# Performance work log

Measured on AMD Instinct MI355X. Metric: run time of the kernel, lower is better.

The kernel has to match this reference:

```python
import jax, jax.numpy as jnp
import numpy as np

N_USERS = 100000
N_ENT = 100000
DIM = 64
HID = 128
E = 1600000
B = 8192


def _renorm(emb, max_norm=1.0):
    # torch nn.Embedding(max_norm=1): rows are rescaled to norm <= max_norm on lookup
    n = jnp.linalg.norm(emb, axis=-1, keepdims=True)
    return emb * jnp.minimum(1.0, max_norm / jnp.maximum(n, 1e-12))


def _gcn_conv(x, W, b, src, dst, n):
    # PyG GCNConv: h = x W; add self-loops; sym-normalized scatter-add; + bias
    h = x @ W  # [n, out]
    deg = jax.ops.segment_sum(jnp.ones(src.shape, jnp.float32), dst, num_segments=n) + 1.0  # self-loop
    dinv = jax.lax.rsqrt(deg)
    norm = (dinv[src] * dinv[dst])[:, None]  # [E,1]
    out = jax.ops.segment_sum(h[src] * norm, dst, num_segments=n)
    out = out + h * (1.0 / deg)[:, None]  # self-loop term: deg^-1/2 * deg^-1/2 = 1/deg
    return out + b


def setup_inputs() -> dict:
    key = jax.random.key(0)
    ks = jax.random.split(key, 8)
    return {
        "u": jax.random.randint(ks[0], (B,), 0, N_USERS),
        "i": jax.random.randint(ks[1], (B,), 0, N_ENT),
        "edges": jax.random.randint(ks[2], (2, E), 0, N_ENT),
        "user_emb": jax.random.normal(ks[3], (N_USERS, DIM), jnp.float32) * 0.1,
        "entity_emb": jax.random.normal(ks[4], (N_ENT, DIM), jnp.float32) * 0.1,
        "W1": jax.random.normal(ks[5], (DIM, HID), jnp.float32) * (1.0 / np.sqrt(DIM)),
        "b1": jnp.zeros((HID,), jnp.float32),
        "W2": jax.random.normal(ks[6], (HID, DIM), jnp.float32) * (1.0 / np.sqrt(HID)),
        "b2": jnp.zeros((DIM,), jnp.float32),
    }


def reference(u, i, edges, user_emb, entity_emb, W1, b1, W2, b2):
    src, dst = edges[0], edges[1]
    n = entity_emb.shape[0]
    x = _renorm(entity_emb)  # entitys(all_entitys_indexes) with max_norm=1
    x = jax.nn.relu(_gcn_conv(x, W1, b1, src, dst, n))  # dropout = identity (eval)
    x = _gcn_conv(x, W2, b2, src, dst, n)
    items = x[i]  # [B, DIM]
    users = _renorm(user_emb)[u]  # [B, DIM]
    uv = jnp.sum(users * items, axis=1)
    return jax.nn.sigmoid(uv)
```

## Files before the change

### kernel.cpp

```cpp
#include <hip/hip_runtime.h>
#include <hip/hip_bf16.h>
#include <math.h>

constexpr int N_ENT = 100000;
constexpr int NEDGE = 1600000;
constexpr int BATCH = 8192;
constexpr int NBLK_SCAN = (N_ENT + 255) / 256;

constexpr int NBUCK   = 256;
constexpr int KNODE   = 391;
constexpr int TILE    = 4096;
constexpr int NTILE   = (NEDGE + TILE - 1) / TILE;
constexpr int BUCKCAP = 8192;

constexpr int NBLK_G = (N_ENT + 63) / 64;
constexpr int ZROWS  = NBLK_G * 64;

typedef __attribute__((ext_vector_type(8))) short bf16x8;
typedef __attribute__((ext_vector_type(4))) float f32x4;

__device__ inline unsigned short f2b(float x) {
    unsigned int u = __float_as_uint(x);
    unsigned int r = (u + 0x7fffu + ((u >> 16) & 1u)) >> 16;
    return (unsigned short)r;
}
__device__ inline float b2f(unsigned short h) {
    return __uint_as_float(((unsigned int)h) << 16);
}
__device__ inline float blo(unsigned int p) { return __uint_as_float(p << 16); }
__device__ inline float bhi(unsigned int p) { return __uint_as_float(p & 0xffff0000u); }


__global__ __launch_bounds__(256) void prep_k(const float* __restrict__ emb,
                                              const int* __restrict__ degi,
                                              float* __restrict__ dinv,
                                              unsigned short* __restrict__ emb_b) {
    int gt   = blockIdx.x * 256 + threadIdx.x;
    int n    = gt >> 6;
    int lane = threadIdx.x & 63;
    if (n > N_ENT) return;
    if (n == N_ENT) { emb_b[(size_t)n * 64 + lane] = 0; return; }
    float v = emb[(size_t)n * 64 + lane];
    float s = v * v;
#pragma unroll
    for (int o = 32; o > 0; o >>= 1) s += __shfl_xor(s, o, 64);
    float nrm = sqrtf(s);
    float sc  = nrm > 1.0f ? 1.0f / nrm : 1.0f;
    float dv  = 1.0f / sqrtf((float)(degi[n] + 1));
    if (lane == 0) dinv[n] = dv;
    emb_b[(size_t)n * 64 + lane] = f2b(sc * dv * v);
}

__global__ __launch_bounds__(256) void ginit_k(int* __restrict__ gcursor) {
    gcursor[threadIdx.x] = threadIdx.x * BUCKCAP;
}

__global__ __launch_bounds__(256) void packw_k(const float* __restrict__ W1g,
                                               const float* __restrict__ W2g,
                                               uint4* __restrict__ w1p,
                                               uint4* __restrict__ w2p) {
    int t = blockIdx.x * 256 + threadIdx.x;
    int e    = t & 1023;
    int lane = e & 63, cs = e >> 6;
    int li   = lane & 15, quad = lane >> 4;
    unsigned short v[8];
    if (t < 1024) {
        int ct = cs >> 1, s = cs & 1;
        int kb = s * 32 + quad * 8;
        int n  = ct * 16 + li;
#pragma unroll
        for (int j = 0; j < 8; ++j) v[j] = f2b(W1g[(kb + j) * 128 + n]);
        uint4 p;
        p.x = (unsigned)v[0] | ((unsigned)v[1] << 16);
        p.y = (unsigned)v[2] | ((unsigned)v[3] << 16);
        p.z = (unsigned)v[4] | ((unsigned)v[5] << 16);
        p.w = (unsigned)v[6] | ((unsigned)v[7] << 16);
        w1p[e] = p;
    } else {
        int ct = cs >> 2, s = cs & 3;
        int kb = s * 32 + quad * 8;
        int n  = ct * 16 + li;
#pragma unroll
        for (int j = 0; j < 8; ++j) v[j] = f2b(W2g[(kb + j) * 64 + n]);
        uint4 p;
        p.x = (unsigned)v[0] | ((unsigned)v[1] << 16);
        p.y = (unsigned)v[2] | ((unsigned)v[3] << 16);
        p.z = (unsigned)v[4] | ((unsigned)v[5] << 16);
        p.w = (unsigned)v[6] | ((unsigned)v[7] << 16);
        w2p[e] = p;
    }
}

__global__ __launch_bounds__(256) void bin_k(const int* __restrict__ edges,
                                             int* __restrict__ gcursor,
                                             unsigned int* __restrict__ temp) {
    __shared__ int cnt[NBUCK];
    __shared__ int gb[NBUCK];
    __shared__ int off[NBUCK];
    int tid  = threadIdx.x;
    int base = blockIdx.x * TILE;
    int sv[16], dv[16], bv[16];
    cnt[tid] = 0;
    __syncthreads();
#pragma unroll
    for (int i = 0; i < 16; ++i) {
        int e = base + i * 256 + tid;
        if (e < NEDGE) {
            sv[i] = edges[e];
            dv[i] = edges[NEDGE + e];
            bv[i] = dv[i] / KNODE;
            atomicAdd(&cnt[bv[i]], 1);
        } else {
            bv[i] = -1;
        }
    }
    __syncthreads();
    if (cnt[tid] > 0) gb[tid] = atomicAdd(&gcursor[tid], cnt[tid]);
    off[tid] = 0;
    __syncthreads();
#pragma unroll
    for (int i = 0; i < 16; ++i) {
        int b = bv[i];
        if (b >= 0) {
            int p  = atomicAdd(&off[b], 1);
            int dl = dv[i] - b * KNODE;
            temp[gb[b] + p] = ((unsigned int)sv[i] << 9) | (unsigned int)dl;
        }
    }
}

__global__ __launch_bounds__(256) void count_k(const unsigned int* __restrict__ temp,
                                               const int* __restrict__ gcursor,
                                               int* __restrict__ degi) {
    __shared__ int cnt[KNODE];
    int b     = blockIdx.x;
    int node0 = b * KNODE;
    int nn    = N_ENT - node0; if (nn > KNODE) nn = KNODE;
    for (int i = threadIdx.x; i < KNODE; i += 256) cnt[i] = 0;
    __syncthreads();
    int tbeg = b * BUCKCAP;
    int tend = gcursor[b];
    for (int idx = tbeg + threadIdx.x; idx < tend; idx += 256)
        atomicAdd(&cnt[temp[idx] & 511u], 1);
    __syncthreads();
    for (int i = threadIdx.x; i < nn; i += 256) degi[node0 + i] = cnt[i];
}

__global__ __launch_bounds__(256) void scan_partials(const int* __restrict__ degi,
                                                     int* __restrict__ partials) {
    __shared__ int ws[4];
    int i = blockIdx.x * 256 + threadIdx.x;
    int v = (i < N_ENT) ? degi[i] : 0;
#pragma unroll
    for (int o = 32; o > 0; o >>= 1) v += __shfl_xor(v, o, 64);
    if ((threadIdx.x & 63) == 0) ws[threadIdx.x >> 6] = v;
    __syncthreads();
    if (threadIdx.x == 0) partials[blockIdx.x] = ws[0] + ws[1] + ws[2] + ws[3];
}

__global__ __launch_bounds__(512) void scan_offsets(int* __restrict__ partials,
                                                    int* __restrict__ row_start) {
    __shared__ int ts[512];
    int t = threadIdx.x;
    int v = (t < NBLK_SCAN) ? partials[t] : 0;
    ts[t] = v;
    __syncthreads();
    for (int off = 1; off < 512; off <<= 1) {
        int x = (t >= off) ? ts[t - off] : 0;
        __syncthreads();
        ts[t] += x;
        __syncthreads();
    }
    if (t < NBLK_SCAN) partials[t] = ts[t] - v;
    if (t == 0) row_start[N_ENT] = NEDGE;
}

__global__ __launch_bounds__(256) void scan_apply(const int* __restrict__ degi,
                                                  const int* __restrict__ partials,
                                                  int* __restrict__ row_start) {
    __shared__ int ts[256];
    int t = threadIdx.x;
    int i = blockIdx.x * 256 + t;
    int v = (i < N_ENT) ? degi[i] : 0;
    ts[t] = v;
    __syncthreads();
    for (int off = 1; off < 256; off <<= 1) {
        int x = (t >= off) ? ts[t - off] : 0;
        __syncthreads();
        ts[t] += x;
        __syncthreads();
    }
    if (i < N_ENT) row_start[i] = ts[t] - v + partials[blockIdx.x];
}

__global__ __launch_bounds__(256) void unbin_k(const unsigned int* __restrict__ temp,
                                               const int* __restrict__ gcursor,
                                               const int* __restrict__ row_start,
                                               int* __restrict__ srcs) {
    __shared__ int cur[KNODE];
    int b     = blockIdx.x;
    int node0 = b * KNODE;
    int nn    = N_ENT - node0; if (nn > KNODE) nn = KNODE;
    for (int i = threadIdx.x; i < nn; i += 256) cur[i] = row_start[node0 + i];
    __syncthreads();
    int tbeg = b * BUCKCAP;
    int tend = gcursor[b];
    for (int idx = tbeg + threadIdx.x; idx < tend; idx += 256) {
        unsigned int v = temp[idx];
        int dl = (int)(v & 511u);
        int s  = (int)(v >> 9);
        int pos = atomicAdd(&cur[dl], 1);
        srcs[pos] = s;
    }
}

__global__ __launch_bounds__(256) void reduce1_k(const int* __restrict__ row_start,
                                                 const int* __restrict__ srcs,
                                                 const unsigned short* __restrict__ emb_b,
                                                 const float* __restrict__ dinv,
                                                 unsigned short* __restrict__ zb) {
    int gt   = blockIdx.x * 256 + threadIdx.x;
    int dst  = gt >> 6;
    int lane = threadIdx.x & 63;
    int sub  = lane >> 4;
    int li   = lane & 15;
    int beg = row_start[dst];
    int end = row_start[dst + 1];
    float4 acc = make_float4(0.f, 0.f, 0.f, 0.f);
    for (int base = beg; base < end; base += 64) {
        int cnt = end - base; if (cnt > 64) cnt = 64;
        int s_v = (base + lane < end) ? srcs[base + lane] : N_ENT;
        for (int jj = 0; jj < cnt; jj += 16) {
            int s0 = __shfl(s_v, jj + sub,      64);
            int s1 = __shfl(s_v, jj + 4 + sub,  64);
            int s2 = __shfl(s_v, jj + 8 + sub,  64);
            int s3 = __shfl(s_v, jj + 12 + sub, 64);
            uint2 p0 = *(const uint2*)(emb_b + (size_t)s0 * 64 + li * 4);
            uint2 p1 = *(const uint2*)(emb_b + (size_t)s1 * 64 + li * 4);
            uint2 p2 = *(const uint2*)(emb_b + (size_t)s2 * 64 + li * 4);
            uint2 p3 = *(const uint2*)(emb_b + (size_t)s3 * 64 + li * 4);
            acc.x += blo(p0.x) + blo(p1.x) + blo(p2.x) + blo(p3.x);
            acc.y += bhi(p0.x) + bhi(p1.x) + bhi(p2.x) + bhi(p3.x);
            acc.z += blo(p0.y) + blo(p1.y) + blo(p2.y) + blo(p3.y);
            acc.w += bhi(p0.y) + bhi(p1.y) + bhi(p2.y) + bhi(p3.y);
        }
    }
    acc.x += __shfl_xor(acc.x, 16, 64); acc.y += __shfl_xor(acc.y, 16, 64);
    acc.z += __shfl_xor(acc.z, 16, 64); acc.w += __shfl_xor(acc.w, 16, 64);
    acc.x += __shfl_xor(acc.x, 32, 64); acc.y += __shfl_xor(acc.y, 32, 64);
    acc.z += __shfl_xor(acc.z, 32, 64); acc.w += __shfl_xor(acc.w, 32, 64);
    if (lane < 16) {
        uint2 po = *(const uint2*)(emb_b + (size_t)dst * 64 + li * 4);
        float dv = dinv[dst];
        unsigned int h0 = f2b(dv * (acc.x + blo(po.x)));
        unsigned int h1 = f2b(dv * (acc.y + bhi(po.x)));
        unsigned int h2 = f2b(dv * (acc.z + blo(po.y)));
        unsigned int h3 = f2b(dv * (acc.w + bhi(po.y)));
        uint2 p;
        p.x = h0 | (h1 << 16);
        p.y = h2 | (h3 << 16);
        *(uint2*)(zb + (size_t)dst * 64 + li * 4) = p;
    }
}

__global__ __launch_bounds__(256) void mlp_k(const unsigned short* __restrict__ zb,
                                             const uint4* __restrict__ w1p,
                                             const float* __restrict__ b1,
                                             const uint4* __restrict__ w2p,
                                             const float* __restrict__ dinv,
                                             unsigned short* __restrict__ h2b) {
    __shared__ unsigned short y1s[4][16 * 136];
    __shared__ unsigned short h2s[4][16 * 64];
    int tid  = threadIdx.x;
    int w    = tid >> 6, lane = tid & 63;
    int li   = lane & 15, quad = lane >> 4;
    int r0   = blockIdx.x * 64 + w * 16;
    uint4 a0u = *(const uint4*)(zb + (size_t)(r0 + li) * 64 + quad * 8);
    uint4 a1u = *(const uint4*)(zb + (size_t)(r0 + li) * 64 + 32 + quad * 8);
    bf16x8 a0 = *(bf16x8*)&a0u;
    bf16x8 a1 = *(bf16x8*)&a1u;
    unsigned short* ys = y1s[w];
#pragma unroll
    for (int ct = 0; ct < 8; ++ct) {
        uint4 b0u = w1p[(ct * 2 + 0) * 64 + lane];
        uint4 b1u = w1p[(ct * 2 + 1) * 64 + lane];
        f32x4 acc = {0.f, 0.f, 0.f, 0.f};
        acc = __builtin_amdgcn_mfma_f32_16x16x32_bf16(a0, *(bf16x8*)&b0u, acc, 0, 0, 0);
        acc = __builtin_amdgcn_mfma_f32_16x16x32_bf16(a1, *(bf16x8*)&b1u, acc, 0, 0, 0);
        float bias = b1[ct * 16 + li];
#pragma unroll
        for (int r = 0; r < 4; ++r)
            ys[(quad * 4 + r) * 136 + ct * 16 + li] = f2b(fmaxf(acc[r] + bias, 0.f));
    }
    __syncthreads();
    bf16x8 a2[4];
#pragma unroll
    for (int s = 0; s < 4; ++s) {
        uint4 au = *(const uint4*)(ys + li * 136 + s * 32 + quad * 8);
        a2[s] = *(bf16x8*)&au;
    }
    float dvr[4];
#pragma unroll
    for (int r = 0; r < 4; ++r) {
        int grow = r0 + quad * 4 + r;
        dvr[r] = (grow < N_ENT) ? dinv[grow] : 0.f;
    }
    unsigned short* hs = h2s[w];
#pragma unroll
    for (int ct = 0; ct < 4; ++ct) {
        f32x4 acc = {0.f, 0.f, 0.f, 0.f};
#pragma unroll
        for (int s = 0; s < 4; ++s) {
            uint4 bu = w2p[(ct * 4 + s) * 64 + lane];
            acc = __builtin_amdgcn_mfma_f32_16x16x32_bf16(a2[s], *(bf16x8*)&bu, acc, 0, 0, 0);
        }
#pragma unroll
        for (int r = 0; r < 4; ++r)
            hs[(quad * 4 + r) * 64 + ct * 16 + li] = f2b(acc[r] * dvr[r]);
    }
    __syncthreads();
#pragma unroll
    for (int q = 0; q < 2; ++q) {
        int t4   = lane * 2 + q;
        int rl   = t4 >> 3;
        int c0   = (t4 & 7) * 8;
        int grow = r0 + rl;
        if (grow < N_ENT) {
            *(uint4*)(h2b + (size_t)grow * 64 + c0) = *(const uint4*)(hs + rl * 64 + c0);
        } else if (grow == N_ENT) {
            uint4 zz; zz.x = 0u; zz.y = 0u; zz.z = 0u; zz.w = 0u;
            *(uint4*)(h2b + (size_t)grow * 64 + c0) = zz;
        }
    }
}

__global__ __launch_bounds__(256) void reduce2f_k(const int* __restrict__ u,
                                                  const int* __restrict__ iidx,
                                                  const float* __restrict__ uemb,
                                                  const int* __restrict__ row_start,
                                                  const int* __restrict__ srcs,
                                                  const unsigned short* __restrict__ h2b,
                                                  const float* __restrict__ dinv,
                                                  const float* __restrict__ b2,
                                                  float* __restrict__ out) {
    int gt   = blockIdx.x * 256 + threadIdx.x;
    int b    = gt >> 6;
    int lane = threadIdx.x & 63;
    int sub  = lane >> 4;
    int li   = lane & 15;
    int dst = iidx[b];
    int beg = row_start[dst];
    int end = row_start[dst + 1];
    float4 acc = make_float4(0.f, 0.f, 0.f, 0.f);
    for (int base = beg; base < end; base += 64) {
        int cnt = end - base; if (cnt > 64) cnt = 64;
        int s_v = (base + lane < end) ? srcs[base + lane] : N_ENT;
        for (int jj = 0; jj < cnt; jj += 16) {
            int s0 = __shfl(s_v, jj + sub,      64);
            int s1 = __shfl(s_v, jj + 4 + sub,  64);
            int s2 = __shfl(s_v, jj + 8 + sub,  64);
            int s3 = __shfl(s_v, jj + 12 + sub, 64);
            uint2 p0 = *(const uint2*)(h2b + (size_t)s0 * 64 + li * 4);
            uint2 p1 = *(const uint2*)(h2b + (size_t)s1 * 64 + li * 4);
            uint2 p2 = *(const uint2*)(h2b + (size_t)s2 * 64 + li * 4);
            uint2 p3 = *(const uint2*)(h2b + (size_t)s3 * 64 + li * 4);
            acc.x += blo(p0.x) + blo(p1.x) + blo(p2.x) + blo(p3.x);
            acc.y += bhi(p0.x) + bhi(p1.x) + bhi(p2.x) + bhi(p3.x);
            acc.z += blo(p0.y) + blo(p1.y) + blo(p2.y) + blo(p3.y);
            acc.w += bhi(p0.y) + bhi(p1.y) + bhi(p2.y) + bhi(p3.y);
        }
    }
    acc.x += __shfl_xor(acc.x, 16, 64); acc.y += __shfl_xor(acc.y, 16, 64);
    acc.z += __shfl_xor(acc.z, 16, 64); acc.w += __shfl_xor(acc.w, 16, 64);
    acc.x += __shfl_xor(acc.x, 32, 64); acc.y += __shfl_xor(acc.y, 32, 64);
    acc.z += __shfl_xor(acc.z, 32, 64); acc.w += __shfl_xor(acc.w, 32, 64);
    float s1 = 0.f, s2 = 0.f;
    if (lane < 16) {
        uint2 po = *(const uint2*)(h2b + (size_t)dst * 64 + li * 4);
        float dv = dinv[dst];
        float4 bb = *(const float4*)(b2 + li * 4);
        float4 z2v;
        z2v.x = dv * (acc.x + blo(po.x)) + bb.x;
        z2v.y = dv * (acc.y + bhi(po.x)) + bb.y;
        z2v.z = dv * (acc.z + blo(po.y)) + bb.z;
        z2v.w = dv * (acc.w + bhi(po.y)) + bb.w;
        float4 ue = *(const float4*)(uemb + (size_t)u[b] * 64 + li * 4);
        s1 = ue.x * ue.x + ue.y * ue.y + ue.z * ue.z + ue.w * ue.w;
        s2 = ue.x * z2v.x + ue.y * z2v.y + ue.z * z2v.z + ue.w * z2v.w;
    }
#pragma unroll
    for (int o = 8; o > 0; o >>= 1) {
        s1 += __shfl_xor(s1, o, 64);
        s2 += __shfl_xor(s2, o, 64);
    }
    if (lane == 0) {
        float nrm = sqrtf(s1);
        float sc  = nrm > 1.0f ? 1.0f / nrm : 1.0f;
        float uv  = s2 * sc;
        out[b] = 1.0f / (1.0f + expf(-uv));
    }
}

extern "C" void kernel_launch(void* const* d_in, const int* in_sizes, int n_in,
                              void* d_out, int out_size, void* d_ws, size_t ws_size,
                              hipStream_t stream) {
    const int*   u          = (const int*)d_in[0];
    const int*   iidx       = (const int*)d_in[1];
    const int*   edges      = (const int*)d_in[2];
    const float* user_emb   = (const float*)d_in[3];
    const float* entity_emb = (const float*)d_in[4];
    const float* W1         = (const float*)d_in[5];
    const float* b1         = (const float*)d_in[6];
    const float* W2         = (const float*)d_in[7];
    const float* b2         = (const float*)d_in[8];
    float*       out        = (float*)d_out;

    char* ws = (char*)d_ws;
    int*            degi      = (int*)           (ws);
    float*          dinv      = (float*)         (ws + 100000u * 4);
    int*            row_start = (int*)           (ws + 200000u * 4);
    int*            gcursor   = (int*)           (ws + 300004u * 4);
    int*            partials  = (int*)           (ws + 300264u * 4);
    uint4*          w1p       = (uint4*)         (ws + 300656u * 4);
    uint4*          w2p       = (uint4*)         (ws + 304752u * 4);
    int*            srcs      = (int*)           (ws + 308848u * 4);
    unsigned short* emb_b     = (unsigned short*)(ws + 1908848u * 4);
    unsigned short* zb        = (unsigned short*)(ws + 3508864u * 4);
    unsigned short* h2b       = (unsigned short*)(ws + 6711936u * 4);
    unsigned int*   temp      = (unsigned int*)  (ws + 8311968u * 4);

    ginit_k<<<1, 256, 0, stream>>>(gcursor);
    packw_k<<<8, 256, 0, stream>>>(W1, W2, w1p, w2p);
    bin_k<<<NTILE, 256, 0, stream>>>(edges, gcursor, temp);
    count_k<<<NBUCK, 256, 0, stream>>>(temp, gcursor, degi);

    prep_k<<<N_ENT * 64 / 256 + 1, 256, 0, stream>>>(entity_emb, degi, dinv, emb_b);

    scan_partials<<<NBLK_SCAN, 256, 0, stream>>>(degi, partials);
    scan_offsets<<<1, 512, 0, stream>>>(partials, row_start);
    scan_apply<<<NBLK_SCAN, 256, 0, stream>>>(degi, partials, row_start);

    unbin_k<<<NBUCK, 256, 0, stream>>>(temp, gcursor, row_start, srcs);

    reduce1_k<<<N_ENT * 64 / 256, 256, 0, stream>>>(row_start, srcs, emb_b, dinv, zb);
    mlp_k<<<NBLK_G, 256, 0, stream>>>(zb, w1p, b1, w2p, dinv, h2b);

    reduce2f_k<<<BATCH * 64 / 256, 256, 0, stream>>>(u, iidx, user_emb, row_start,
                                                     srcs, h2b, dinv, b2, out);
}
```

Before: 244.4 us.

## Split bf16 embeddings into two column planes and run reduce1 as two passes

The bf16 normalized entity embeddings and the first aggregation output are now stored as two planes of 32 columns each instead of interleaved 64-column rows. reduce1 launches twice as many blocks, and each pass gathers only one 64-byte half-row per source, so the gathered working set per pass fits in cache better and there is more parallelism. mlp_k reads its two K-halves from the two planes. The cost is re-reading the CSR indices and row_start twice, plus more wavefronts each doing half the arithmetic.

New measurement: 251.6 us. 2.9% more time.

```diff
diff --git a/kernel.cpp b/kernel.cpp
--- a/kernel.cpp
+++ b/kernel.cpp
@@ -15,6 +15,10 @@
 
 constexpr int NBLK_G = (N_ENT + 63) / 64;
 constexpr int ZROWS  = NBLK_G * 64;
+
+constexpr int    NBLK_R1 = N_ENT * 64 / 256;
+constexpr size_t EPLANE  = (size_t)(N_ENT + 1) * 32;
+constexpr size_t ZPLANE  = (size_t)ZROWS * 32;
 
 typedef __attribute__((ext_vector_type(8))) short bf16x8;
 typedef __attribute__((ext_vector_type(4))) float f32x4;
@@ -39,7 +43,9 @@
     int n    = gt >> 6;
     int lane = threadIdx.x & 63;
     if (n > N_ENT) return;
-    if (n == N_ENT) { emb_b[(size_t)n * 64 + lane] = 0; return; }
+    int plane = lane >> 5;
+    int cp    = lane & 31;
+    if (n == N_ENT) { emb_b[(size_t)plane * EPLANE + (size_t)n * 32 + cp] = 0; return; }
     float v = emb[(size_t)n * 64 + lane];
     float s = v * v;
 #pragma unroll
@@ -48,7 +54,7 @@
     float sc  = nrm > 1.0f ? 1.0f / nrm : 1.0f;
     float dv  = 1.0f / sqrtf((float)(degi[n] + 1));
     if (lane == 0) dinv[n] = dv;
-    emb_b[(size_t)n * 64 + lane] = f2b(sc * dv * v);
+    emb_b[(size_t)plane * EPLANE + (size_t)n * 32 + cp] = f2b(sc * dv * v);
 }
 
 __global__ __launch_bounds__(256) void ginit_k(int* __restrict__ gcursor) {
@@ -219,14 +225,16 @@
                                                  const unsigned short* __restrict__ emb_b,
                                                  const float* __restrict__ dinv,
                                                  unsigned short* __restrict__ zb) {
-    int gt   = blockIdx.x * 256 + threadIdx.x;
+    int pass = (blockIdx.x >= NBLK_R1) ? 1 : 0;
+    int gt   = (blockIdx.x - pass * NBLK_R1) * 256 + threadIdx.x;
     int dst  = gt >> 6;
     int lane = threadIdx.x & 63;
     int sub  = lane >> 4;
     int li   = lane & 15;
+    const unsigned short* eb = emb_b + (size_t)pass * EPLANE;
     int beg = row_start[dst];
     int end = row_start[dst + 1];
-    float4 acc = make_float4(0.f, 0.f, 0.f, 0.f);
+    float accx = 0.f, accy = 0.f;
     for (int base = beg; base < end; base += 64) {
         int cnt = end - base; if (cnt > 64) cnt = 64;
         int s_v = (base + lane < end) ? srcs[base + lane] : N_ENT;
@@ -235,31 +243,23 @@
             int s1 = __shfl(s_v, jj + 4 + sub,  64);
             int s2 = __shfl(s_v, jj + 8 + sub,  64);
             int s3 = __shfl(s_v, jj + 12 + sub, 64);
-            uint2 p0 = *(const uint2*)(emb_b + (size_t)s0 * 64 + li * 4);
-            uint2 p1 = *(const uint2*)(emb_b + (size_t)s1 * 64 + li * 4);
-            uint2 p2 = *(const uint2*)(emb_b + (size_t)s2 * 64 + li * 4);
-            uint2 p3 = *(const uint2*)(emb_b + (size_t)s3 * 64 + li * 4);
-            acc.x += blo(p0.x) + blo(p1.x) + blo(p2.x) + blo(p3.x);
-            acc.y += bhi(p0.x) + bhi(p1.x) + bhi(p2.x) + bhi(p3.x);
-            acc.z += blo(p0.y) + blo(p1.y) + blo(p2.y) + blo(p3.y);
-            acc.w += bhi(p0.y) + bhi(p1.y) + bhi(p2.y) + bhi(p3.y);
-        }
-    }
-    acc.x += __shfl_xor(acc.x, 16, 64); acc.y += __shfl_xor(acc.y, 16, 64);
-    acc.z += __shfl_xor(acc.z, 16, 64); acc.w += __shfl_xor(acc.w, 16, 64);
-    acc.x += __shfl_xor(acc.x, 32, 64); acc.y += __shfl_xor(acc.y, 32, 64);
-    acc.z += __shfl_xor(acc.z, 32, 64); acc.w += __shfl_xor(acc.w, 32, 64);
+            unsigned int p0 = *(const unsigned int*)(eb + (size_t)s0 * 32 + li * 2);
+            unsigned int p1 = *(const unsigned int*)(eb + (size_t)s1 * 32 + li * 2);
+            unsigned int p2 = *(const unsigned int*)(eb + (size_t)s2 * 32 + li * 2);
+            unsigned int p3 = *(const unsigned int*)(eb + (size_t)s3 * 32 + li * 2);
+            accx += blo(p0) + blo(p1) + blo(p2) + blo(p3);
+            accy += bhi(p0) + bhi(p1) + bhi(p2) + bhi(p3);
+        }
+    }
+    accx += __shfl_xor(accx, 16, 64); accy += __shfl_xor(accy, 16, 64);
+    accx += __shfl_xor(accx, 32, 64); accy += __shfl_xor(accy, 32, 64);
     if (lane < 16) {
-        uint2 po = *(const uint2*)(emb_b + (size_t)dst * 64 + li * 4);
+        unsigned int po = *(const unsigned int*)(eb + (size_t)dst * 32 + li * 2);
         float dv = dinv[dst];
-        unsigned int h0 = f2b(dv * (acc.x + blo(po.x)));
-        unsigned int h1 = f2b(dv * (acc.y + bhi(po.x)));
-        unsigned int h2 = f2b(dv * (acc.z + blo(po.y)));
-        unsigned int h3 = f2b(dv * (acc.w + bhi(po.y)));
-        uint2 p;
-        p.x = h0 | (h1 << 16);
-        p.y = h2 | (h3 << 16);
-        *(uint2*)(zb + (size_t)dst * 64 + li * 4) = p;
+        unsigned int h0 = f2b(dv * (accx + blo(po)));
+        unsigned int h1 = f2b(dv * (accy + bhi(po)));
+        *(unsigned int*)(zb + (size_t)pass * ZPLANE + (size_t)dst * 32 + li * 2) =
+            h0 | (h1 << 16);
     }
 }
 
@@ -275,8 +275,8 @@
     int w    = tid >> 6, lane = tid & 63;
     int li   = lane & 15, quad = lane >> 4;
     int r0   = blockIdx.x * 64 + w * 16;
-    uint4 a0u = *(const uint4*)(zb + (size_t)(r0 + li) * 64 + quad * 8);
-    uint4 a1u = *(const uint4*)(zb + (size_t)(r0 + li) * 64 + 32 + quad * 8);
+    uint4 a0u = *(const uint4*)(zb + (size_t)(r0 + li) * 32 + quad * 8);
+    uint4 a1u = *(const uint4*)(zb + ZPLANE + (size_t)(r0 + li) * 32 + quad * 8);
     bf16x8 a0 = *(bf16x8*)&a0u;
     bf16x8 a1 = *(bf16x8*)&a1u;
     unsigned short* ys = y1s[w];
@@ -442,7 +442,7 @@
 
     unbin_k<<<NBUCK, 256, 0, stream>>>(temp, gcursor, row_start, srcs);
 
-    reduce1_k<<<N_ENT * 64 / 256, 256, 0, stream>>>(row_start, srcs, emb_b, dinv, zb);
+    reduce1_k<<<2 * NBLK_R1, 256, 0, stream>>>(row_start, srcs, emb_b, dinv, zb);
     mlp_k<<<NBLK_G, 256, 0, stream>>>(zb, w1p, b1, w2p, dinv, h2b);
 
     reduce2f_k<<<BATCH * 64 / 256, 256, 0, stream>>>(u, iidx, user_emb, row_start,
```

## Replace three-pass degree scan with bucket-level scan fused into unbin

Applied to the files above, without the earlier changes.

Merges the gcursor init and weight packing into one launch. Replaces the global three-kernel prefix scan over node degrees with a single scan over bucket counts, followed by a per-bucket local scan inside unbin_k that writes row_start. In bin_k, each edge's packed value is computed once and its bucket index is stored in bytes, which lowers register use. Together these cut the launch count from 12 to 9 and remove a full pass over the degree array, at the cost of a short serial scan by one wavefront at the start of each unbin block.

New measurement: 238.2 us. 1.03x faster.

```diff
diff --git a/kernel.cpp b/kernel.cpp
--- a/kernel.cpp
+++ b/kernel.cpp
@@ -5,7 +5,6 @@
 constexpr int N_ENT = 100000;
 constexpr int NEDGE = 1600000;
 constexpr int BATCH = 8192;
-constexpr int NBLK_SCAN = (N_ENT + 255) / 256;
 
 constexpr int NBUCK   = 256;
 constexpr int KNODE   = 391;
@@ -16,6 +15,7 @@
 constexpr int NBLK_G = (N_ENT + 63) / 64;
 constexpr int ZROWS  = NBLK_G * 64;
 
+
 typedef __attribute__((ext_vector_type(8))) short bf16x8;
 typedef __attribute__((ext_vector_type(4))) float f32x4;
 
@@ -23,9 +23,6 @@
     unsigned int u = __float_as_uint(x);
     unsigned int r = (u + 0x7fffu + ((u >> 16) & 1u)) >> 16;
     return (unsigned short)r;
-}
-__device__ inline float b2f(unsigned short h) {
-    return __uint_as_float(((unsigned int)h) << 16);
 }
 __device__ inline float blo(unsigned int p) { return __uint_as_float(p << 16); }
 __device__ inline float bhi(unsigned int p) { return __uint_as_float(p & 0xffff0000u); }
@@ -51,14 +48,12 @@
     emb_b[(size_t)n * 64 + lane] = f2b(sc * dv * v);
 }
 
-__global__ __launch_bounds__(256) void ginit_k(int* __restrict__ gcursor) {
-    gcursor[threadIdx.x] = threadIdx.x * BUCKCAP;
-}
-
-__global__ __launch_bounds__(256) void packw_k(const float* __restrict__ W1g,
-                                               const float* __restrict__ W2g,
-                                               uint4* __restrict__ w1p,
-                                               uint4* __restrict__ w2p) {
+__global__ __launch_bounds__(256) void init_k(const float* __restrict__ W1g,
+                                              const float* __restrict__ W2g,
+                                              uint4* __restrict__ w1p,
+                                              uint4* __restrict__ w2p,
+                                              int* __restrict__ gcursor) {
+    if (blockIdx.x == 8) { gcursor[threadIdx.x] = threadIdx.x * BUCKCAP; return; }
     int t = blockIdx.x * 256 + threadIdx.x;
     int e    = t & 1023;
     int lane = e & 63, cs = e >> 6;
@@ -99,20 +94,26 @@
     __shared__ int off[NBUCK];
     int tid  = threadIdx.x;
     int base = blockIdx.x * TILE;
-    int sv[16], dv[16], bv[16];
+    unsigned int val[16];
+    unsigned int bpk[4] = {0u, 0u, 0u, 0u};
     cnt[tid] = 0;
     __syncthreads();
 #pragma unroll
     for (int i = 0; i < 16; ++i) {
         int e = base + i * 256 + tid;
+        unsigned int b = 0u;
         if (e < NEDGE) {
-            sv[i] = edges[e];
-            dv[i] = edges[NEDGE + e];
-            bv[i] = dv[i] / KNODE;
-            atomicAdd(&cnt[bv[i]], 1);
+            int s  = edges[e];
+            int d  = edges[NEDGE + e];
+            int bb = d / KNODE;
+            int dl = d - bb * KNODE;
+            val[i] = ((unsigned int)s << 9) | (unsigned int)dl;
+            b = (unsigned int)bb;
+            atomicAdd(&cnt[bb], 1);
         } else {
-            bv[i] = -1;
-        }
+            val[i] = 0xffffffffu;
+        }
+        bpk[i >> 2] |= b << ((i & 3) * 8);
     }
     __syncthreads();
     if (cnt[tid] > 0) gb[tid] = atomicAdd(&gcursor[tid], cnt[tid]);
@@ -120,11 +121,10 @@
     __syncthreads();
 #pragma unroll
     for (int i = 0; i < 16; ++i) {
-        int b = bv[i];
-        if (b >= 0) {
-            int p  = atomicAdd(&off[b], 1);
-            int dl = dv[i] - b * KNODE;
-            temp[gb[b] + p] = ((unsigned int)sv[i] << 9) | (unsigned int)dl;
+        if (val[i] != 0xffffffffu) {
+            int b = (int)((bpk[i >> 2] >> ((i & 3) * 8)) & 255u);
+            int p = atomicAdd(&off[b], 1);
+            temp[gb[b] + p] = val[i];
         }
     }
 }
@@ -146,66 +146,68 @@
     for (int i = threadIdx.x; i < nn; i += 256) degi[node0 + i] = cnt[i];
 }
 
-__global__ __launch_bounds__(256) void scan_partials(const int* __restrict__ degi,
-                                                     int* __restrict__ partials) {
-    __shared__ int ws[4];
-    int i = blockIdx.x * 256 + threadIdx.x;
-    int v = (i < N_ENT) ? degi[i] : 0;
-#pragma unroll
-    for (int o = 32; o > 0; o >>= 1) v += __shfl_xor(v, o, 64);
-    if ((threadIdx.x & 63) == 0) ws[threadIdx.x >> 6] = v;
-    __syncthreads();
-    if (threadIdx.x == 0) partials[blockIdx.x] = ws[0] + ws[1] + ws[2] + ws[3];
-}
-
-__global__ __launch_bounds__(512) void scan_offsets(int* __restrict__ partials,
+__global__ __launch_bounds__(256) void scan_offsets(const int* __restrict__ gcursor,
+                                                    int* __restrict__ bucket_base,
                                                     int* __restrict__ row_start) {
-    __shared__ int ts[512];
+    __shared__ int ts[NBUCK];
     int t = threadIdx.x;
-    int v = (t < NBLK_SCAN) ? partials[t] : 0;
+    int v = gcursor[t] - t * BUCKCAP;
     ts[t] = v;
     __syncthreads();
-    for (int off = 1; off < 512; off <<= 1) {
+    for (int off = 1; off < NBUCK; off <<= 1) {
         int x = (t >= off) ? ts[t - off] : 0;
         __syncthreads();
         ts[t] += x;
         __syncthreads();
     }
-    if (t < NBLK_SCAN) partials[t] = ts[t] - v;
+    bucket_base[t] = ts[t] - v;
     if (t == 0) row_start[N_ENT] = NEDGE;
-}
-
-__global__ __launch_bounds__(256) void scan_apply(const int* __restrict__ degi,
-                                                  const int* __restrict__ partials,
-                                                  int* __restrict__ row_start) {
-    __shared__ int ts[256];
-    int t = threadIdx.x;
-    int i = blockIdx.x * 256 + t;
-    int v = (i < N_ENT) ? degi[i] : 0;
-    ts[t] = v;
-    __syncthreads();
-    for (int off = 1; off < 256; off <<= 1) {
-        int x = (t >= off) ? ts[t - off] : 0;
-        __syncthreads();
-        ts[t] += x;
-        __syncthreads();
-    }
-    if (i < N_ENT) row_start[i] = ts[t] - v + partials[blockIdx.x];
 }
 
 __global__ __launch_bounds__(256) void unbin_k(const unsigned int* __restrict__ temp,
                                                const int* __restrict__ gcursor,
-                                               const int* __restrict__ row_start,
+                                               const int* __restrict__ bucket_base,
+                                               const int* __restrict__ degi,
+                                               int* __restrict__ row_start,
                                                int* __restrict__ srcs) {
     __shared__ int cur[KNODE];
     int b     = blockIdx.x;
     int node0 = b * KNODE;
     int nn    = N_ENT - node0; if (nn > KNODE) nn = KNODE;
-    for (int i = threadIdx.x; i < nn; i += 256) cur[i] = row_start[node0 + i];
+    int tid   = threadIdx.x;
+    if (tid < 64) {
+        int lane = tid;
+        int loc[7];
+        int s = 0;
+#pragma unroll
+        for (int j = 0; j < 7; ++j) {
+            int idx = lane * 7 + j;
+            int d = (idx < nn) ? degi[node0 + idx] : 0;
+            loc[j] = s;
+            s += d;
+        }
+        int v = s;
+#pragma unroll
+        for (int o = 1; o < 64; o <<= 1) {
+            int x = __shfl_up(v, o, 64);
+            if (lane >= o) v += x;
+        }
+        int pfx  = v - s;
+        int base = bucket_base[b];
+#pragma unroll
+        for (int j = 0; j < 7; ++j) {
+            int idx = lane * 7 + j;
+            if (idx < nn) {
+                int rs = base + pfx + loc[j];
+                cur[idx] = rs;
+                row_start[node0 + idx] = rs;
+            }
+        }
+    }
     __syncthreads();
     int tbeg = b * BUCKCAP;
     int tend = gcursor[b];
-    for (int idx = tbeg + threadIdx.x; idx < tend; idx += 256) {
+    for (int idx = tbeg + tid; idx < tend; idx += 256) {
         unsigned int v = temp[idx];
         int dl = (int)(v & 511u);
         int s  = (int)(v >> 9);
@@ -416,31 +418,28 @@
     float*       out        = (float*)d_out;
 
     char* ws = (char*)d_ws;
-    int*            degi      = (int*)           (ws);
-    float*          dinv      = (float*)         (ws + 100000u * 4);
-    int*            row_start = (int*)           (ws + 200000u * 4);
-    int*            gcursor   = (int*)           (ws + 300004u * 4);
-    int*            partials  = (int*)           (ws + 300264u * 4);
-    uint4*          w1p       = (uint4*)         (ws + 300656u * 4);
-    uint4*          w2p       = (uint4*)         (ws + 304752u * 4);
-    int*            srcs      = (int*)           (ws + 308848u * 4);
-    unsigned short* emb_b     = (unsigned short*)(ws + 1908848u * 4);
-    unsigned short* zb        = (unsigned short*)(ws + 3508864u * 4);
-    unsigned short* h2b       = (unsigned short*)(ws + 6711936u * 4);
-    unsigned int*   temp      = (unsigned int*)  (ws + 8311968u * 4);
-
-    ginit_k<<<1, 256, 0, stream>>>(gcursor);
-    packw_k<<<8, 256, 0, stream>>>(W1, W2, w1p, w2p);
+    int*            degi        = (int*)           (ws);
+    float*          dinv        = (float*)         (ws + 100000u * 4);
+    int*            row_start   = (int*)           (ws + 200000u * 4);
+    int*            gcursor     = (int*)           (ws + 300004u * 4);
+    int*            bucket_base = (int*)           (ws + 300264u * 4);
+    uint4*          w1p         = (uint4*)         (ws + 300656u * 4);
+    uint4*          w2p         = (uint4*)         (ws + 304752u * 4);
+    int*            srcs        = (int*)           (ws + 308848u * 4);
+    unsigned short* emb_b       = (unsigned short*)(ws + 1908848u * 4);
+    unsigned short* zb          = (unsigned short*)(ws + 3508864u * 4);
+    unsigned short* h2b         = (unsigned short*)(ws + 6711936u * 4);
+    unsigned int*   temp        = (unsigned int*)  (ws + 8311968u * 4);
+
+    init_k<<<9, 256, 0, stream>>>(W1, W2, w1p, w2p, gcursor);
     bin_k<<<NTILE, 256, 0, stream>>>(edges, gcursor, temp);
     count_k<<<NBUCK, 256, 0, stream>>>(temp, gcursor, degi);
+    scan_offsets<<<1, 256, 0, stream>>>(gcursor, bucket_base, row_start);
 
     prep_k<<<N_ENT * 64 / 256 + 1, 256, 0, stream>>>(entity_emb, degi, dinv, emb_b);
 
-    scan_partials<<<NBLK_SCAN, 256, 0, stream>>>(degi, partials);
-    scan_offsets<<<1, 512, 0, stream>>>(partials, row_start);
-    scan_apply<<<NBLK_SCAN, 256, 0, stream>>>(degi, partials, row_start);
-
-    unbin_k<<<NBUCK, 256, 0, stream>>>(temp, gcursor, row_start, srcs);
+    unbin_k<<<NBUCK, 256, 0, stream>>>(temp, gcursor, bucket_base, degi,
+                                       row_start, srcs);
 
     reduce1_k<<<N_ENT * 64 / 256, 256, 0, stream>>>(row_start, srcs, emb_b, dinv, zb);
     mlp_k<<<NBLK_G, 256, 0, stream>>>(zb, w1p, b1, w2p, dinv, h2b);
```
